# Optimization experiments

Hardware: AMD Instinct MI355X
Metric: run time of the kernel (lower is better)

Reference implementation:

```python
import jax, jax.numpy as jnp
import numpy as np

HID1, HID2 = 512, 1024   # enc_chans = [hidden_dim * 2**i for i in range(num_layers)]
CODE_DIM, N_TOK = 512, 8192
N_RES = 3


def conv1d(x, w, b, stride=1, pad=1):
    # x: [B,C,T], w: [O,I,K], b: [O]
    y = jax.lax.conv_general_dilated(x, w, (stride,), [(pad, pad)],
                                     dimension_numbers=("NCH", "OIH", "NCH"))
    return y + b[None, :, None]


def setup_inputs() -> dict:
    key = jax.random.key(0)
    ks = jax.random.split(key, 16)
    s = 0.02
    inp = {
        "x":   jax.random.normal(ks[0], (16, 80, 2048), jnp.float32),
        "w1":  jax.random.normal(ks[1], (HID1, 80, 3), jnp.float32) * s,
        "b1":  jnp.zeros((HID1,), jnp.float32),
        "w2":  jax.random.normal(ks[2], (HID2, HID1, 3), jnp.float32) * s,
        "b2":  jnp.zeros((HID2,), jnp.float32),
        "rwa": jax.random.normal(ks[3], (N_RES, HID2, HID2, 3), jnp.float32) * s,
        "rba": jnp.zeros((N_RES, HID2), jnp.float32),
        "rwb": jax.random.normal(ks[4], (N_RES, HID2, HID2, 3), jnp.float32) * s,
        "rbb": jnp.zeros((N_RES, HID2), jnp.float32),
        "rwc": jax.random.normal(ks[5], (N_RES, HID2, HID2, 1), jnp.float32) * s,
        "rbc": jnp.zeros((N_RES, HID2), jnp.float32),
        "wf":  jax.random.normal(ks[6], (CODE_DIM, HID2, 1), jnp.float32) * s,
        "bf":  jnp.zeros((CODE_DIM,), jnp.float32),
        "codebook": jax.random.normal(ks[7], (CODE_DIM, N_TOK), jnp.float32),
    }
    return inp


def _encode(x, w1, b1, w2, b2, rwa, rba, rwb, rbb, rwc, rbc, wf, bf):
    h = jax.nn.relu(conv1d(x, w1, b1, stride=2, pad=1))   # [B,512,T/2]
    h = jax.nn.relu(conv1d(h, w2, b2, stride=2, pad=1))   # [B,1024,T/4]
    for i in range(N_RES):                                # ResBlock: conv3-relu-conv3-relu-conv1 + x
        r = jax.nn.relu(conv1d(h, rwa[i], rba[i], 1, 1))
        r = jax.nn.relu(conv1d(r, rwb[i], rbb[i], 1, 1))
        r = conv1d(r, rwc[i], rbc[i], 1, 0)
        h = h + r
    return conv1d(h, wf, bf, 1, 0)                        # [B,512,T/4]


def reference(x, w1, b1, w2, b2, rwa, rba, rwb, rbb, rwc, rbc, wf, bf, codebook):
    lat = _encode(x, w1, b1, w2, b2, rwa, rba, rwb, rbb, rwc, rbc, wf, bf)
    B, D, Tq = lat.shape
    f = lat.transpose(0, 2, 1).reshape(-1, D)             # [B*Tq, 512]
    # squared-distance argmin against codebook [512, 8192]
    dist = (jnp.sum(f * f, axis=1, keepdims=True)
            - 2.0 * (f @ codebook)
            + jnp.sum(codebook * codebook, axis=0)[None, :])
    codes = jnp.argmin(dist, axis=-1).reshape(B, Tq)      # int codes [B, T/4]
    return codes
```

## Files before the change

kernel.cpp:

```cpp
#include <hip/hip_runtime.h>
#include <cstdint>

#define BATCH   16
#define T_IN    2048
#define HID1    512
#define HID2    1024
#define T1      1024
#define T2      512
#define CODE_DIM 512
#define N_TOK   8192
#define N_RES   3
#define N_ROWS  (BATCH * T2)

typedef short bf16x8 __attribute__((ext_vector_type(8)));
typedef float f32x4  __attribute__((ext_vector_type(4)));
typedef unsigned short u16;

union B128 { int4 i; bf16x8 b; };

__device__ __forceinline__ unsigned splitpack(float v) {
    unsigned r  = __float_as_uint(v);
    unsigned hi = (r + 0x7FFFu + ((r >> 16) & 1u)) >> 16;
    float    res = v - __uint_as_float(hi << 16);
    unsigned rl = __float_as_uint(res);
    unsigned lo = (rl + 0x7FFFu + ((rl >> 16) & 1u)) >> 16;
    return hi | (lo << 16);
}
__device__ __forceinline__ float bf2f(u16 b) { return __uint_as_float(((unsigned)b) << 16); }
__device__ __forceinline__ int swz(int row) { return (row ^ (row >> 2)) & 3; }

template<int TAPS, int S, int WR, bool WPRE, bool RELU, bool ADD>
__global__ __launch_bounds__(256, 2)
void conv_mfma(const u16* __restrict__ xH, const u16* __restrict__ xL,
               const float* __restrict__ wraw,
               const u16* __restrict__ wHp, const u16* __restrict__ wLp,
               const float* __restrict__ bias,
               const u16* __restrict__ addH, const u16* __restrict__ addL,
               u16* __restrict__ oH, u16* __restrict__ oL,
               int Cin, int Cout, int Tin, int Tout, int ntc)
{
    constexpr int BM = WR * 2, BN = 128;
    constexpr int PAD  = (TAPS == 3) ? 1 : 0;
    constexpr int SPAN = BM * S + TAPS - S;
    constexpr int MF   = WR / 16;

    __shared__ int4 sXh[SPAN][4], sXl[SPAN][4];
    __shared__ int4 sWh[BN][4],  sWl[BN][4];

    const int tid  = threadIdx.x;
    const int lane = tid & 63, wid = tid >> 6;
    const int wm = wid >> 1, wn = wid & 1;
    const int l15 = lane & 15, l4 = lane >> 4;

    const int bid = blockIdx.x;
    const int nt = bid % ntc, mt = bid / ntc;
    const int R0 = mt * BM, o0 = nt * BN;
    const int b  = R0 / Tout, t0 = R0 % Tout;
    const int tbase = t0 * S - PAD;

    f32x4 acc[MF][4] = {};

    const u16* bxH = xH + (size_t)b * Tin * Cin;
    const u16* bxL = xL + (size_t)b * Tin * Cin;

    for (int c0 = 0; c0 < Cin; c0 += 32) {
        for (int tap = 0; tap < TAPS; ++tap) {
            __syncthreads();
            if (tap == 0) {
                for (int r = tid; r < SPAN; r += 256) {
                    const int t = tbase + r;
                    const int s = swz(r);
                    if (t >= 0 && t < Tin) {
                        const int4* pH = (const int4*)(bxH + (size_t)t * Cin + c0);
                        const int4* pL = (const int4*)(bxL + (size_t)t * Cin + c0);
#pragma unroll
                        for (int j = 0; j < 4; ++j) sXh[r][j ^ s] = pH[j];
#pragma unroll
                        for (int j = 0; j < 4; ++j) sXl[r][j ^ s] = pL[j];
                    } else {
                        const int4 z = {0, 0, 0, 0};
#pragma unroll
                        for (int j = 0; j < 4; ++j) { sXh[r][j] = z; sXl[r][j] = z; }
                    }
                }
            }
            if constexpr (WPRE) {
                const int row = tid & 127, half = tid >> 7;
                const int s = swz(row);
                const size_t base = ((size_t)tap * Cout + (o0 + row)) * Cin + c0 + half * 16;
                const int4* pH = (const int4*)(wHp + base);
                const int4* pL = (const int4*)(wLp + base);
                sWh[row][(half * 2 + 0) ^ s] = pH[0];
                sWh[row][(half * 2 + 1) ^ s] = pH[1];
                sWl[row][(half * 2 + 0) ^ s] = pL[0];
                sWl[row][(half * 2 + 1) ^ s] = pL[1];
            } else {
                const int row = tid >> 1, half = tid & 1;
                const int s = swz(row);
                const float* wp = wraw + ((size_t)(o0 + row) * Cin + (c0 + half * 16)) * TAPS + tap;
                unsigned p[16];
#pragma unroll
                for (int j = 0; j < 16; ++j) p[j] = splitpack(wp[(size_t)j * TAPS]);
                int4 h0, h1, l0, l1;
                h0.x = (int)((p[0]&0xFFFFu)|(p[1]<<16));   h0.y = (int)((p[2]&0xFFFFu)|(p[3]<<16));
                h0.z = (int)((p[4]&0xFFFFu)|(p[5]<<16));   h0.w = (int)((p[6]&0xFFFFu)|(p[7]<<16));
                h1.x = (int)((p[8]&0xFFFFu)|(p[9]<<16));   h1.y = (int)((p[10]&0xFFFFu)|(p[11]<<16));
                h1.z = (int)((p[12]&0xFFFFu)|(p[13]<<16)); h1.w = (int)((p[14]&0xFFFFu)|(p[15]<<16));
                l0.x = (int)((p[0]>>16)|(p[1]&0xFFFF0000u));   l0.y = (int)((p[2]>>16)|(p[3]&0xFFFF0000u));
                l0.z = (int)((p[4]>>16)|(p[5]&0xFFFF0000u));   l0.w = (int)((p[6]>>16)|(p[7]&0xFFFF0000u));
                l1.x = (int)((p[8]>>16)|(p[9]&0xFFFF0000u));   l1.y = (int)((p[10]>>16)|(p[11]&0xFFFF0000u));
                l1.z = (int)((p[12]>>16)|(p[13]&0xFFFF0000u)); l1.w = (int)((p[14]>>16)|(p[15]&0xFFFF0000u));
                sWh[row][(half * 2 + 0) ^ s] = h0;  sWh[row][(half * 2 + 1) ^ s] = h1;
                sWl[row][(half * 2 + 0) ^ s] = l0;  sWl[row][(half * 2 + 1) ^ s] = l1;
            }
            __syncthreads();

            B128 bh[4], bl[4];
#pragma unroll
            for (int nf = 0; nf < 4; ++nf) {
                const int orow = wn * 64 + nf * 16 + l15;
                const int sl = l4 ^ swz(orow);
                bh[nf].i = sWh[orow][sl];  bl[nf].i = sWl[orow][sl];
            }
#pragma unroll
            for (int mf = 0; mf < MF; ++mf) {
                const int r = (wm * WR + mf * 16 + l15) * S + tap;
                const int sl = l4 ^ swz(r);
                B128 ah, al;
                ah.i = sXh[r][sl];  al.i = sXl[r][sl];
#pragma unroll
                for (int nf = 0; nf < 4; ++nf) {
                    acc[mf][nf] = __builtin_amdgcn_mfma_f32_16x16x32_bf16(ah.b, bh[nf].b, acc[mf][nf], 0, 0, 0);
                    acc[mf][nf] = __builtin_amdgcn_mfma_f32_16x16x32_bf16(ah.b, bl[nf].b, acc[mf][nf], 0, 0, 0);
                    acc[mf][nf] = __builtin_amdgcn_mfma_f32_16x16x32_bf16(al.b, bh[nf].b, acc[mf][nf], 0, 0, 0);
                }
            }
        }
    }

#pragma unroll
    for (int nf = 0; nf < 4; ++nf) {
        const int o = o0 + wn * 64 + nf * 16 + l15;
        const float bv = bias[o];
#pragma unroll
        for (int mf = 0; mf < MF; ++mf) {
#pragma unroll
            for (int rg = 0; rg < 4; ++rg) {
                const int Rl = wm * WR + mf * 16 + l4 * 4 + rg;
                const size_t idx = (size_t)(R0 + Rl) * Cout + o;
                float v = acc[mf][nf][rg] + bv;
                if constexpr (ADD)  v += bf2f(addH[idx]) + bf2f(addL[idx]);
                if constexpr (RELU) v = fmaxf(v, 0.f);
                const unsigned p = splitpack(v);
                oH[idx] = (u16)(p & 0xFFFFu);
                oL[idx] = (u16)(p >> 16);
            }
        }
    }
}

__global__ void prep_x(const float* __restrict__ x, u16* __restrict__ xH, u16* __restrict__ xL)
{
    const int id = blockIdx.x * 256 + threadIdx.x;
    const int b = id >> 11, t = id & 2047;
    const float* src = x + (size_t)b * 80 * 2048 + t;
    u16* dH = xH + (size_t)id * 96;
    u16* dL = xL + (size_t)id * 96;
    for (int c = 0; c < 96; ++c) {
        const float v = (c < 80) ? src[(size_t)c * 2048] : 0.f;
        const unsigned p = splitpack(v);
        dH[c] = (u16)(p & 0xFFFFu);
        dL[c] = (u16)(p >> 16);
    }
}

__global__ void prep_w(const float* __restrict__ w, u16* __restrict__ wH, u16* __restrict__ wL,
                       int O, int CinR, int CinP, int TAPS)
{
    const int id = blockIdx.x * 256 + threadIdx.x;
    if (id >= O * CinP) return;
    const int o = id / CinP, c = id % CinP;
    for (int t = 0; t < TAPS; ++t) {
        const float v = (c < CinR) ? w[((size_t)o * CinR + c) * TAPS + t] : 0.f;
        const unsigned p = splitpack(v);
        const size_t dst = ((size_t)t * O + o) * CinP + c;
        wH[dst] = (u16)(p & 0xFFFFu);
        wL[dst] = (u16)(p >> 16);
    }
}

__global__ void prep_cb(const float* __restrict__ cb, u16* __restrict__ cH, u16* __restrict__ cL)
{
    __shared__ float tile[32][33];
    const int jb = blockIdx.x * 32, db = blockIdx.y * 32;
    const int c = threadIdx.x & 31, r = threadIdx.x >> 5;
    for (int rr = r; rr < 32; rr += 8)
        tile[rr][c] = cb[(size_t)(db + rr) * N_TOK + jb + c];
    __syncthreads();
    for (int rr = r; rr < 32; rr += 8) {
        const unsigned p = splitpack(tile[c][rr]);
        const size_t dst = (size_t)(jb + rr) * CODE_DIM + db + c;
        cH[dst] = (u16)(p & 0xFFFFu);
        cL[dst] = (u16)(p >> 16);
    }
}

__global__ void cnorm_kernel(const float* __restrict__ cb, float* __restrict__ cnorm)
{
    const int j = blockIdx.x * 256 + threadIdx.x;
    float s = 0.f;
#pragma unroll 8
    for (int d = 0; d < CODE_DIM; ++d) {
        const float v = cb[(size_t)d * N_TOK + j];
        s += v * v;
    }
    cnorm[j] = s;
}

__global__ __launch_bounds__(256, 2)
void vq_mfma(const u16* __restrict__ latH, const u16* __restrict__ latL,
             const u16* __restrict__ cbH, const u16* __restrict__ cbL,
             const float* __restrict__ cnorm,
             float* __restrict__ pval, int* __restrict__ pidx)
{
    __shared__ int4 sXh[256][4], sXl[256][4];
    __shared__ int4 sWh[128][4], sWl[128][4];

    const int tid  = threadIdx.x;
    const int lane = tid & 63, wid = tid >> 6;
    const int wm = wid >> 1, wn = wid & 1;
    const int l15 = lane & 15, l4 = lane >> 4;
    const int R0 = blockIdx.x * 256;
    const int o0 = blockIdx.y * 128;

    f32x4 acc[8][4] = {};

    for (int c0 = 0; c0 < CODE_DIM; c0 += 32) {
        __syncthreads();
        {
            const int s = swz(tid);
            const int4* pH = (const int4*)(latH + (size_t)(R0 + tid) * CODE_DIM + c0);
            const int4* pL = (const int4*)(latL + (size_t)(R0 + tid) * CODE_DIM + c0);
#pragma unroll
            for (int j = 0; j < 4; ++j) sXh[tid][j ^ s] = pH[j];
#pragma unroll
            for (int j = 0; j < 4; ++j) sXl[tid][j ^ s] = pL[j];
        }
        {
            const int row = tid & 127, half = tid >> 7;
            const int s = swz(row);
            const size_t base = (size_t)(o0 + row) * CODE_DIM + c0 + half * 16;
            const int4* pH = (const int4*)(cbH + base);
            const int4* pL = (const int4*)(cbL + base);
            sWh[row][(half * 2 + 0) ^ s] = pH[0];
            sWh[row][(half * 2 + 1) ^ s] = pH[1];
            sWl[row][(half * 2 + 0) ^ s] = pL[0];
            sWl[row][(half * 2 + 1) ^ s] = pL[1];
        }
        __syncthreads();

        B128 bh[4], bl[4];
#pragma unroll
        for (int nf = 0; nf < 4; ++nf) {
            const int orow = wn * 64 + nf * 16 + l15;
            const int sl = l4 ^ swz(orow);
            bh[nf].i = sWh[orow][sl];  bl[nf].i = sWl[orow][sl];
        }
#pragma unroll
        for (int mf = 0; mf < 8; ++mf) {
            const int r = wm * 128 + mf * 16 + l15;
            const int sl = l4 ^ swz(r);
            B128 ah, al;
            ah.i = sXh[r][sl];  al.i = sXl[r][sl];
#pragma unroll
            for (int nf = 0; nf < 4; ++nf) {
                acc[mf][nf] = __builtin_amdgcn_mfma_f32_16x16x32_bf16(ah.b, bh[nf].b, acc[mf][nf], 0, 0, 0);
                acc[mf][nf] = __builtin_amdgcn_mfma_f32_16x16x32_bf16(ah.b, bl[nf].b, acc[mf][nf], 0, 0, 0);
                acc[mf][nf] = __builtin_amdgcn_mfma_f32_16x16x32_bf16(al.b, bh[nf].b, acc[mf][nf], 0, 0, 0);
            }
        }
    }

    float cn[4]; int jb[4];
#pragma unroll
    for (int nf = 0; nf < 4; ++nf) {
        jb[nf] = o0 + wn * 64 + nf * 16 + l15;
        cn[nf] = cnorm[jb[nf]];
    }
    const int slice = blockIdx.y * 2 + wn;
#pragma unroll
    for (int mf = 0; mf < 8; ++mf) {
#pragma unroll
        for (int rg = 0; rg < 4; ++rg) {
            float bv = -3.4e38f; int bj = 0;
#pragma unroll
            for (int nf = 0; nf < 4; ++nf) {
                const float v = 2.f * acc[mf][nf][rg] - cn[nf];
                if (v > bv) { bv = v; bj = jb[nf]; }
            }
#pragma unroll
            for (int m = 1; m < 16; m <<= 1) {
                const float ov = __shfl_xor(bv, m, 64);
                const int   oj = __shfl_xor(bj, m, 64);
                if (ov > bv || (ov == bv && oj < bj)) { bv = ov; bj = oj; }
            }
            if (l15 == 0) {
                const int R = R0 + wm * 128 + mf * 16 + l4 * 4 + rg;
                pval[(size_t)slice * N_ROWS + R] = bv;
                pidx[(size_t)slice * N_ROWS + R] = bj;
            }
        }
    }
}

__global__ void vq_merge(const float* __restrict__ pval, const int* __restrict__ pidx,
                         int* __restrict__ out)
{
    const int row = blockIdx.x * 256 + threadIdx.x;
    float bv = pval[row]; int bj = pidx[row];
    for (int s = 1; s < 128; ++s) {
        const float v = pval[(size_t)s * N_ROWS + row];
        const int   j = pidx[(size_t)s * N_ROWS + row];
        if (v > bv || (v == bv && j < bj)) { bv = v; bj = j; }
    }
    out[row] = bj;
}

extern "C" void kernel_launch(void* const* d_in, const int* in_sizes, int n_in,
                              void* d_out, int out_size, void* d_ws, size_t ws_size,
                              hipStream_t stream)
{
    const float* x   = (const float*)d_in[0];
    const float* w1  = (const float*)d_in[1];
    const float* b1  = (const float*)d_in[2];
    const float* w2  = (const float*)d_in[3];
    const float* b2  = (const float*)d_in[4];
    const float* rwa = (const float*)d_in[5];
    const float* rba = (const float*)d_in[6];
    const float* rwb = (const float*)d_in[7];
    const float* rbb = (const float*)d_in[8];
    const float* rwc = (const float*)d_in[9];
    const float* rbc = (const float*)d_in[10];
    const float* wf  = (const float*)d_in[11];
    const float* bf  = (const float*)d_in[12];
    const float* cb  = (const float*)d_in[13];

    char* W = (char*)d_ws;
    u16* h1H = (u16*)(W + 0);          u16* h1L = (u16*)(W + 16777216);
    u16* h2H = (u16*)(W + 33554432);   u16* h2L = (u16*)(W + 50331648);
    u16* r2H = (u16*)(W + 67108864);   u16* r2L = (u16*)(W + 83886080);
    u16* r1H = h1H;                    u16* r1L = h1L;
    u16* latH = h1H;                   u16* latL = h1L;
    u16* xPH  = (u16*)(W + 67108864);  u16* xPL  = (u16*)(W + 73400320);
    u16* w1PH = (u16*)(W + 79691776);  u16* w1PL = (u16*)(W + 79986688);
    u16* w2PH = (u16*)(W + 80281600);  u16* w2PL = (u16*)(W + 83427328);
    u16* cbTH = (u16*)(W + 67108864);  u16* cbTL = (u16*)(W + 75497472);
    float* CN = (float*)(W + 83886080);
    float* PV = (float*)(W + 83918848);
    int*   PI = (int*)(W + 88113152);
    const bool WPRE = ws_size >= (size_t)132120576;
    u16* raPH = (u16*)(W + 100663296); u16* raPL = (u16*)(W + 106954752);
    u16* rbPH = (u16*)(W + 113246208); u16* rbPL = (u16*)(W + 119537664);
    u16* rcPH = (u16*)(W + 125829120); u16* rcPL = (u16*)(W + 127926272);
    u16* wfPH = (u16*)(W + 130023424); u16* wfPL = (u16*)(W + 131072000);

    prep_x<<<BATCH * T_IN / 256, 256, 0, stream>>>(x, xPH, xPL);
    prep_w<<<(HID1 * 96 + 255) / 256, 256, 0, stream>>>(w1, w1PH, w1PL, HID1, 80, 96, 3);
    prep_w<<<(HID2 * HID1 + 255) / 256, 256, 0, stream>>>(w2, w2PH, w2PL, HID2, HID1, HID1, 3);

    conv_mfma<3, 2, 64, true, true, false><<<512, 256, 0, stream>>>(
        xPH, xPL, nullptr, w1PH, w1PL, b1, nullptr, nullptr, h1H, h1L,
        96, HID1, T_IN, T1, 4);
    conv_mfma<3, 2, 64, true, true, false><<<512, 256, 0, stream>>>(
        h1H, h1L, nullptr, w2PH, w2PL, b2, nullptr, nullptr, h2H, h2L,
        HID1, HID2, T1, T2, 8);

    for (int i = 0; i < N_RES; ++i) {
        const float* wa = rwa + (size_t)i * HID2 * HID2 * 3;
        const float* wb = rwb + (size_t)i * HID2 * HID2 * 3;
        const float* wc = rwc + (size_t)i * HID2 * HID2;
        if (WPRE) {
            prep_w<<<(HID2 * HID2 + 255) / 256, 256, 0, stream>>>(wa, raPH, raPL, HID2, HID2, HID2, 3);
            prep_w<<<(HID2 * HID2 + 255) / 256, 256, 0, stream>>>(wb, rbPH, rbPL, HID2, HID2, HID2, 3);
            prep_w<<<(HID2 * HID2 + 255) / 256, 256, 0, stream>>>(wc, rcPH, rcPL, HID2, HID2, HID2, 1);
            conv_mfma<3, 1, 64, true, true, false><<<512, 256, 0, stream>>>(
                h2H, h2L, nullptr, raPH, raPL, rba + (size_t)i * HID2, nullptr, nullptr,
                r1H, r1L, HID2, HID2, T2, T2, 8);
            conv_mfma<3, 1, 64, true, true, false><<<512, 256, 0, stream>>>(
                r1H, r1L, nullptr, rbPH, rbPL, rbb + (size_t)i * HID2, nullptr, nullptr,
                r2H, r2L, HID2, HID2, T2, T2, 8);
            conv_mfma<1, 1, 64, true, false, true><<<512, 256, 0, stream>>>(
                r2H, r2L, nullptr, rcPH, rcPL, rbc + (size_t)i * HID2, h2H, h2L,
                h2H, h2L, HID2, HID2, T2, T2, 8);
        } else {
            conv_mfma<3, 1, 64, false, true, false><<<512, 256, 0, stream>>>(
                h2H, h2L, wa, nullptr, nullptr, rba + (size_t)i * HID2, nullptr, nullptr,
                r1H, r1L, HID2, HID2, T2, T2, 8);
            conv_mfma<3, 1, 64, false, true, false><<<512, 256, 0, stream>>>(
                r1H, r1L, wb, nullptr, nullptr, rbb + (size_t)i * HID2, nullptr, nullptr,
                r2H, r2L, HID2, HID2, T2, T2, 8);
            conv_mfma<1, 1, 64, false, false, true><<<512, 256, 0, stream>>>(
                r2H, r2L, wc, nullptr, nullptr, rbc + (size_t)i * HID2, h2H, h2L,
                h2H, h2L, HID2, HID2, T2, T2, 8);
        }
    }

    if (WPRE) {
        prep_w<<<(CODE_DIM * HID2 + 255) / 256, 256, 0, stream>>>(wf, wfPH, wfPL, CODE_DIM, HID2, HID2, 1);
        conv_mfma<1, 1, 32, true, false, false><<<512, 256, 0, stream>>>(
            h2H, h2L, nullptr, wfPH, wfPL, bf, nullptr, nullptr, latH, latL,
            HID2, CODE_DIM, T2, T2, 4);
    } else {
        conv_mfma<1, 1, 32, false, false, false><<<512, 256, 0, stream>>>(
            h2H, h2L, wf, nullptr, nullptr, bf, nullptr, nullptr, latH, latL,
            HID2, CODE_DIM, T2, T2, 4);
    }

    prep_cb<<<dim3(N_TOK / 32, CODE_DIM / 32), 256, 0, stream>>>(cb, cbTH, cbTL);
    cnorm_kernel<<<N_TOK / 256, 256, 0, stream>>>(cb, CN);
    vq_mfma<<<dim3(N_ROWS / 256, N_TOK / 128), 256, 0, stream>>>(latH, latL, cbTH, cbTL, CN, PV, PI);
    vq_merge<<<N_ROWS / 256, 256, 0, stream>>>(PV, PI, (int*)d_out);
}
```

Baseline: 2.176 ms.

## Add register-prefetched conv kernel and prefetch in VQ kernel

```diff
diff --git a/kernel.cpp b/kernel.cpp
--- a/kernel.cpp
+++ b/kernel.cpp
@@ -28,6 +28,141 @@
 }
 __device__ __forceinline__ float bf2f(u16 b) { return __uint_as_float(((unsigned)b) << 16); }
 __device__ __forceinline__ int swz(int row) { return (row ^ (row >> 2)) & 3; }
+
+template<int TAPS, int S, int WR, bool RELU, bool ADD>
+__global__ __launch_bounds__(256, 2)
+void conv_mfma2(const u16* __restrict__ xH, const u16* __restrict__ xL,
+                const u16* __restrict__ wHp, const u16* __restrict__ wLp,
+                const float* __restrict__ bias,
+                const u16* __restrict__ addH, const u16* __restrict__ addL,
+                u16* __restrict__ oH, u16* __restrict__ oL,
+                int Cin, int Cout, int Tin, int Tout, int ntc)
+{
+    constexpr int BM = WR * 2, BN = 128;
+    constexpr int PAD  = (TAPS == 3) ? 1 : 0;
+    constexpr int SPAN = BM * S + TAPS - S;
+    constexpr int MF   = WR / 16;
+    static_assert(SPAN <= 256, "one staged row per thread");
+
+    __shared__ int4 sXh[SPAN][4], sXl[SPAN][4];
+    __shared__ int4 sWh[TAPS][BN][4], sWl[TAPS][BN][4];
+
+    const int tid  = threadIdx.x;
+    const int lane = tid & 63, wid = tid >> 6;
+    const int wm = wid >> 1, wn = wid & 1;
+    const int l15 = lane & 15, l4 = lane >> 4;
+
+    const int bid = blockIdx.x;
+    const int nt = bid % ntc, mt = bid / ntc;
+    const int R0 = mt * BM, o0 = nt * BN;
+    const int b  = R0 / Tout, t0 = R0 % Tout;
+    const int tbase = t0 * S - PAD;
+
+    const u16* bxH = xH + (size_t)b * Tin * Cin;
+    const u16* bxL = xL + (size_t)b * Tin * Cin;
+
+    f32x4 acc[MF][4] = {};
+
+    int4 pXh[4], pXl[4], pW[TAPS][4];
+    const int  xt     = tbase + tid;
+    const bool xvalid = (tid < SPAN) && (xt >= 0) && (xt < Tin);
+    const int  wrow   = tid >> 1, whalf = tid & 1;
+
+    auto loadX = [&](int c0) {
+        if (xvalid) {
+            const int4* pH = (const int4*)(bxH + (size_t)xt * Cin + c0);
+            const int4* pL = (const int4*)(bxL + (size_t)xt * Cin + c0);
+#pragma unroll
+            for (int j = 0; j < 4; ++j) { pXh[j] = pH[j]; pXl[j] = pL[j]; }
+        } else {
+            const int4 z = {0, 0, 0, 0};
+#pragma unroll
+            for (int j = 0; j < 4; ++j) { pXh[j] = z; pXl[j] = z; }
+        }
+    };
+    auto loadW = [&](int c0) {
+#pragma unroll
+        for (int u = 0; u < TAPS; ++u) {
+            const size_t base = ((size_t)u * Cout + (o0 + wrow)) * Cin + c0 + whalf * 16;
+            const int4* pH = (const int4*)(wHp + base);
+            const int4* pL = (const int4*)(wLp + base);
+            pW[u][0] = pH[0]; pW[u][1] = pH[1];
+            pW[u][2] = pL[0]; pW[u][3] = pL[1];
+        }
+    };
+    auto storeLDS = [&]() {
+        if (tid < SPAN) {
+            const int s = swz(tid);
+#pragma unroll
+            for (int j = 0; j < 4; ++j) sXh[tid][j ^ s] = pXh[j];
+#pragma unroll
+            for (int j = 0; j < 4; ++j) sXl[tid][j ^ s] = pXl[j];
+        }
+        const int s = swz(wrow);
+#pragma unroll
+        for (int u = 0; u < TAPS; ++u) {
+            sWh[u][wrow][(whalf * 2 + 0) ^ s] = pW[u][0];
+            sWh[u][wrow][(whalf * 2 + 1) ^ s] = pW[u][1];
+            sWl[u][wrow][(whalf * 2 + 0) ^ s] = pW[u][2];
+            sWl[u][wrow][(whalf * 2 + 1) ^ s] = pW[u][3];
+        }
+    };
+
+    loadX(0); loadW(0);
+    for (int c0 = 0; c0 < Cin; c0 += 32) {
+        __syncthreads();
+        storeLDS();
+        __syncthreads();
+        if (c0 + 32 < Cin) { loadX(c0 + 32); loadW(c0 + 32); }
+
+        __builtin_amdgcn_s_setprio(1);
+#pragma unroll
+        for (int tap = 0; tap < TAPS; ++tap) {
+            B128 bh[4], bl[4];
+#pragma unroll
+            for (int nf = 0; nf < 4; ++nf) {
+                const int orow = wn * 64 + nf * 16 + l15;
+                const int sl = l4 ^ swz(orow);
+                bh[nf].i = sWh[tap][orow][sl];
+                bl[nf].i = sWl[tap][orow][sl];
+            }
+#pragma unroll
+            for (int mf = 0; mf < MF; ++mf) {
+                const int r = (wm * WR + mf * 16 + l15) * S + tap;
+                const int sl = l4 ^ swz(r);
+                B128 ah, al;
+                ah.i = sXh[r][sl];  al.i = sXl[r][sl];
+#pragma unroll
+                for (int nf = 0; nf < 4; ++nf) {
+                    acc[mf][nf] = __builtin_amdgcn_mfma_f32_16x16x32_bf16(ah.b, bh[nf].b, acc[mf][nf], 0, 0, 0);
+                    acc[mf][nf] = __builtin_amdgcn_mfma_f32_16x16x32_bf16(ah.b, bl[nf].b, acc[mf][nf], 0, 0, 0);
+                    acc[mf][nf] = __builtin_amdgcn_mfma_f32_16x16x32_bf16(al.b, bh[nf].b, acc[mf][nf], 0, 0, 0);
+                }
+            }
+        }
+        __builtin_amdgcn_s_setprio(0);
+    }
+
+#pragma unroll
+    for (int nf = 0; nf < 4; ++nf) {
+        const int o = o0 + wn * 64 + nf * 16 + l15;
+        const float bv = bias[o];
+#pragma unroll
+        for (int mf = 0; mf < MF; ++mf) {
+#pragma unroll
+            for (int rg = 0; rg < 4; ++rg) {
+                const int Rl = wm * WR + mf * 16 + l4 * 4 + rg;
+                const size_t idx = (size_t)(R0 + Rl) * Cout + o;
+                float v = acc[mf][nf][rg] + bv;
+                if constexpr (ADD)  v += bf2f(addH[idx]) + bf2f(addL[idx]);
+                if constexpr (RELU) v = fmaxf(v, 0.f);
+                const unsigned p = splitpack(v);
+                oH[idx] = (u16)(p & 0xFFFFu);
+                oL[idx] = (u16)(p >> 16);
+            }
+        }
+    }
+}
 
 template<int TAPS, int S, int WR, bool WPRE, bool RELU, bool ADD>
 __global__ __launch_bounds__(256, 2)
@@ -235,30 +370,44 @@
 
     f32x4 acc[8][4] = {};
 
+    int4 pXh[4], pXl[4], pW[4];
+    const u16* xrowH = latH + (size_t)(R0 + tid) * CODE_DIM;
+    const u16* xrowL = latL + (size_t)(R0 + tid) * CODE_DIM;
+    const int wrow = tid >> 1, whalf = tid & 1;
+    const u16* wrowH = cbH + (size_t)(o0 + wrow) * CODE_DIM + whalf * 16;
+    const u16* wrowL = cbL + (size_t)(o0 + wrow) * CODE_DIM + whalf * 16;
+
+    auto loadAll = [&](int c0) {
+        const int4* pH = (const int4*)(xrowH + c0);
+        const int4* pL = (const int4*)(xrowL + c0);
+#pragma unroll
+        for (int j = 0; j < 4; ++j) { pXh[j] = pH[j]; pXl[j] = pL[j]; }
+        pW[0] = ((const int4*)(wrowH + c0))[0];
+        pW[1] = ((const int4*)(wrowH + c0))[1];
+        pW[2] = ((const int4*)(wrowL + c0))[0];
+        pW[3] = ((const int4*)(wrowL + c0))[1];
+    };
+    auto storeLDS = [&]() {
+        const int s = swz(tid);
+#pragma unroll
+        for (int j = 0; j < 4; ++j) sXh[tid][j ^ s] = pXh[j];
+#pragma unroll
+        for (int j = 0; j < 4; ++j) sXl[tid][j ^ s] = pXl[j];
+        const int ws = swz(wrow);
+        sWh[wrow][(whalf * 2 + 0) ^ ws] = pW[0];
+        sWh[wrow][(whalf * 2 + 1) ^ ws] = pW[1];
+        sWl[wrow][(whalf * 2 + 0) ^ ws] = pW[2];
+        sWl[wrow][(whalf * 2 + 1) ^ ws] = pW[3];
+    };
+
+    loadAll(0);
     for (int c0 = 0; c0 < CODE_DIM; c0 += 32) {
         __syncthreads();
-        {
-            const int s = swz(tid);
-            const int4* pH = (const int4*)(latH + (size_t)(R0 + tid) * CODE_DIM + c0);
-            const int4* pL = (const int4*)(latL + (size_t)(R0 + tid) * CODE_DIM + c0);
-#pragma unroll
-            for (int j = 0; j < 4; ++j) sXh[tid][j ^ s] = pH[j];
-#pragma unroll
-            for (int j = 0; j < 4; ++j) sXl[tid][j ^ s] = pL[j];
-        }
-        {
-            const int row = tid & 127, half = tid >> 7;
-            const int s = swz(row);
-            const size_t base = (size_t)(o0 + row) * CODE_DIM + c0 + half * 16;
-            const int4* pH = (const int4*)(cbH + base);
-            const int4* pL = (const int4*)(cbL + base);
-            sWh[row][(half * 2 + 0) ^ s] = pH[0];
-            sWh[row][(half * 2 + 1) ^ s] = pH[1];
-            sWl[row][(half * 2 + 0) ^ s] = pL[0];
-            sWl[row][(half * 2 + 1) ^ s] = pL[1];
-        }
+        storeLDS();
         __syncthreads();
-
+        if (c0 + 32 < CODE_DIM) loadAll(c0 + 32);
+
+        __builtin_amdgcn_s_setprio(1);
         B128 bh[4], bl[4];
 #pragma unroll
         for (int nf = 0; nf < 4; ++nf) {
@@ -279,6 +428,7 @@
                 acc[mf][nf] = __builtin_amdgcn_mfma_f32_16x16x32_bf16(al.b, bh[nf].b, acc[mf][nf], 0, 0, 0);
             }
         }
+        __builtin_amdgcn_s_setprio(0);
     }
 
     float cn[4]; int jb[4];
@@ -368,31 +518,43 @@
     prep_w<<<(HID1 * 96 + 255) / 256, 256, 0, stream>>>(w1, w1PH, w1PL, HID1, 80, 96, 3);
     prep_w<<<(HID2 * HID1 + 255) / 256, 256, 0, stream>>>(w2, w2PH, w2PL, HID2, HID1, HID1, 3);
 
-    conv_mfma<3, 2, 64, true, true, false><<<512, 256, 0, stream>>>(
-        xPH, xPL, nullptr, w1PH, w1PL, b1, nullptr, nullptr, h1H, h1L,
-        96, HID1, T_IN, T1, 4);
-    conv_mfma<3, 2, 64, true, true, false><<<512, 256, 0, stream>>>(
-        h1H, h1L, nullptr, w2PH, w2PL, b2, nullptr, nullptr, h2H, h2L,
-        HID1, HID2, T1, T2, 8);
-
-    for (int i = 0; i < N_RES; ++i) {
-        const float* wa = rwa + (size_t)i * HID2 * HID2 * 3;
-        const float* wb = rwb + (size_t)i * HID2 * HID2 * 3;
-        const float* wc = rwc + (size_t)i * HID2 * HID2;
-        if (WPRE) {
-            prep_w<<<(HID2 * HID2 + 255) / 256, 256, 0, stream>>>(wa, raPH, raPL, HID2, HID2, HID2, 3);
-            prep_w<<<(HID2 * HID2 + 255) / 256, 256, 0, stream>>>(wb, rbPH, rbPL, HID2, HID2, HID2, 3);
-            prep_w<<<(HID2 * HID2 + 255) / 256, 256, 0, stream>>>(wc, rcPH, rcPL, HID2, HID2, HID2, 1);
-            conv_mfma<3, 1, 64, true, true, false><<<512, 256, 0, stream>>>(
-                h2H, h2L, nullptr, raPH, raPL, rba + (size_t)i * HID2, nullptr, nullptr,
+    if (WPRE) {
+        conv_mfma2<3, 2, 32, true, false><<<1024, 256, 0, stream>>>(
+            xPH, xPL, w1PH, w1PL, b1, nullptr, nullptr, h1H, h1L, 96, HID1, T_IN, T1, 4);
+        conv_mfma2<3, 2, 32, true, false><<<1024, 256, 0, stream>>>(
+            h1H, h1L, w2PH, w2PL, b2, nullptr, nullptr, h2H, h2L, HID1, HID2, T1, T2, 8);
+        for (int i = 0; i < N_RES; ++i) {
+            prep_w<<<(HID2 * HID2 + 255) / 256, 256, 0, stream>>>(
+                rwa + (size_t)i * 3145728, raPH, raPL, HID2, HID2, HID2, 3);
+            prep_w<<<(HID2 * HID2 + 255) / 256, 256, 0, stream>>>(
+                rwb + (size_t)i * 3145728, rbPH, rbPL, HID2, HID2, HID2, 3);
+            prep_w<<<(HID2 * HID2 + 255) / 256, 256, 0, stream>>>(
+                rwc + (size_t)i * 1048576, rcPH, rcPL, HID2, HID2, HID2, 1);
+            conv_mfma2<3, 1, 64, true, false><<<512, 256, 0, stream>>>(
+                h2H, h2L, raPH, raPL, rba + (size_t)i * HID2, nullptr, nullptr,
                 r1H, r1L, HID2, HID2, T2, T2, 8);
-            conv_mfma<3, 1, 64, true, true, false><<<512, 256, 0, stream>>>(
-                r1H, r1L, nullptr, rbPH, rbPL, rbb + (size_t)i * HID2, nullptr, nullptr,
+            conv_mfma2<3, 1, 64, true, false><<<512, 256, 0, stream>>>(
+                r1H, r1L, rbPH, rbPL, rbb + (size_t)i * HID2, nullptr, nullptr,
                 r2H, r2L, HID2, HID2, T2, T2, 8);
-            conv_mfma<1, 1, 64, true, false, true><<<512, 256, 0, stream>>>(
-                r2H, r2L, nullptr, rcPH, rcPL, rbc + (size_t)i * HID2, h2H, h2L,
+            conv_mfma2<1, 1, 64, false, true><<<512, 256, 0, stream>>>(
+                r2H, r2L, rcPH, rcPL, rbc + (size_t)i * HID2, h2H, h2L,
                 h2H, h2L, HID2, HID2, T2, T2, 8);
-        } else {
+        }
+        prep_w<<<(CODE_DIM * HID2 + 255) / 256, 256, 0, stream>>>(wf, wfPH, wfPL, CODE_DIM, HID2, HID2, 1);
+        conv_mfma2<1, 1, 32, false, false><<<512, 256, 0, stream>>>(
+            h2H, h2L, wfPH, wfPL, bf, nullptr, nullptr, latH, latL,
+            HID2, CODE_DIM, T2, T2, 4);
+    } else {
+        conv_mfma<3, 2, 64, true, true, false><<<512, 256, 0, stream>>>(
+            xPH, xPL, nullptr, w1PH, w1PL, b1, nullptr, nullptr, h1H, h1L,
+            96, HID1, T_IN, T1, 4);
+        conv_mfma<3, 2, 64, true, true, false><<<512, 256, 0, stream>>>(
+            h1H, h1L, nullptr, w2PH, w2PL, b2, nullptr, nullptr, h2H, h2L,
+            HID1, HID2, T1, T2, 8);
+        for (int i = 0; i < N_RES; ++i) {
+            const float* wa = rwa + (size_t)i * HID2 * HID2 * 3;
+            const float* wb = rwb + (size_t)i * HID2 * HID2 * 3;
+            const float* wc = rwc + (size_t)i * HID2 * HID2;
             conv_mfma<3, 1, 64, false, true, false><<<512, 256, 0, stream>>>(
                 h2H, h2L, wa, nullptr, nullptr, rba + (size_t)i * HID2, nullptr, nullptr,
                 r1H, r1L, HID2, HID2, T2, T2, 8);
@@ -403,14 +565,6 @@
                 r2H, r2L, wc, nullptr, nullptr, rbc + (size_t)i * HID2, h2H, h2L,
                 h2H, h2L, HID2, HID2, T2, T2, 8);
         }
-    }
-
-    if (WPRE) {
-        prep_w<<<(CODE_DIM * HID2 + 255) / 256, 256, 0, stream>>>(wf, wfPH, wfPL, CODE_DIM, HID2, HID2, 1);
-        conv_mfma<1, 1, 32, true, false, false><<<512, 256, 0, stream>>>(
-            h2H, h2L, nullptr, wfPH, wfPL, bf, nullptr, nullptr, latH, latL,
-            HID2, CODE_DIM, T2, T2, 4);
-    } else {
         conv_mfma<1, 1, 32, false, false, false><<<512, 256, 0, stream>>>(
             h2H, h2L, wf, nullptr, nullptr, bf, nullptr, nullptr, latH, latL,
             HID2, CODE_DIM, T2, T2, 4);
```

Result: slower. 3.879 ms (+78.3%).
